# Performance work log

Measured on AMD Instinct MI355X. Metric: run time of the kernel, lower is better.

The kernel has to match this reference:

```python
import jax, jax.numpy as jnp
import numpy as np

BS, N, E = 16, 1024, 262144
IN_DIM, HID, OUT, NREL, NBASES = 3072, 512, 128, 8, 4
N_LAYERS = 3


def setup_inputs() -> dict:
    key = jax.random.key(0)
    ks = jax.random.split(key, 10)
    tot = BS * N
    return {
        "h": jax.random.normal(ks[0], (BS, N, IN_DIM), jnp.float32),
        "src": jax.random.randint(ks[1], (E,), 0, tot, jnp.int32),
        "dst": jax.random.randint(ks[2], (E,), 0, tot, jnp.int32),
        "r": jax.random.randint(ks[3], (E,), 0, NREL, jnp.int32),
        "norm": jax.random.uniform(ks[4], (E,), jnp.float32),
        "W_elmo": jax.random.normal(ks[5], (IN_DIM, 256), jnp.float32) * 0.02,
        "b_elmo": jnp.zeros((256,), jnp.float32),
        "comp": jax.random.normal(ks[6], (NREL, NBASES), jnp.float32),
        "V": jax.random.normal(ks[7], (NBASES, HID, HID), jnp.float32) * 0.04,
        "b_gcn": jnp.zeros((HID,), jnp.float32),
        "W_out": jax.random.normal(ks[8], (HID, OUT), jnp.float32) * 0.04,
        "b_out": jnp.zeros((OUT,), jnp.float32),
    }


def reference(h, src, dst, r, norm, W_elmo, b_elmo, comp, V, b_gcn, W_out, b_out):
    bs, n, _ = h.shape
    tot = bs * n
    # elmo_fnn + relu, then concat with zeros -> gnn_h_dim = 512
    x = jax.nn.relu(h @ W_elmo + b_elmo)                 # [bs, N, 256]
    x = jnp.concatenate([x, jnp.zeros_like(x)], axis=-1)  # [bs, N, 512]
    x = x.reshape(tot, HID)                               # flattened batched-graph nodes

    coef = comp[r]  # [E, NBASES] per-edge relation coefficients (basis decomposition)
    nb = V.shape[0]
    for _ in range(N_LAYERS):  # shared RelGraphConv applied repeatedly
        hs = x[src]  # [E, HID] gather source node features per edge
        # message m_e = h_src @ (sum_b comp[r_e, b] * V_b); loop over small fixed basis count
        msg = coef[:, 0:1] * (hs @ V[0])
        for b in range(1, nb):
            msg = msg + coef[:, b:b + 1] * (hs @ V[b])
        msg = msg * norm[:, None]  # per-edge norm weighting
        x = jax.ops.segment_sum(msg, dst, num_segments=tot)  # scatter-aggregate to dst
        x = jax.nn.relu(x + b_gcn)  # bias + activation (no self-loop, dropout=0)

    x = x.reshape(bs, n, HID).mean(axis=1)  # mean over nodes per graph
    logits = x @ W_out + b_out
    return jax.nn.softmax(logits, axis=-1)
```

## Files before the change

kernel.cpp:

```cpp
#include <hip/hip_runtime.h>

typedef unsigned short u16;
typedef unsigned int   u32;
typedef u16   u16x4 __attribute__((ext_vector_type(4)));
typedef u16   u16x8 __attribute__((ext_vector_type(8)));
typedef short s16x8 __attribute__((ext_vector_type(8)));
typedef u32   u32x4 __attribute__((ext_vector_type(4)));
typedef float f32x4 __attribute__((ext_vector_type(4)));

__device__ __forceinline__ float bf2f(u16 u) {
    u32 x = ((u32)u) << 16;
    return __builtin_bit_cast(float, x);
}
__device__ __forceinline__ u16 f2bf(float f) {
    u32 u = __builtin_bit_cast(u32, f);
    u32 r = u + 0x7FFFu + ((u >> 16) & 1u);
    return (u16)(r >> 16);
}
__device__ __forceinline__ u32 cvtpk(float a, float b) {
    u32 r;
    asm("v_cvt_pk_bf16_f32 %0, %1, %2" : "=v"(r) : "v"(a), "v"(b));
    return r;
}

__device__ __forceinline__ void gload16(const void* g, void* lds) {
    __builtin_amdgcn_global_load_lds((const __attribute__((address_space(1))) void*)g,
                                     (__attribute__((address_space(3))) void*)lds, 16, 0, 0);
}

#define TOT   16384
#define HID   512
#define NRELS 8
#define EDGES 262144
#define INDIM 3072
#define NOUT  128
#define NGRAPH 16
#define NODESPER 1024
#define EKSPLIT 4

#define OFF_XB     ((size_t)0)
#define OFF_Y      (OFF_XB + 16777216)
#define OFF_WCT    (OFF_Y + 134217728)
#define OFF_WET    (OFF_WCT + 4194304)
#define OFF_CNT    (OFF_WET + 1572864)
#define OFF_ROWPTR (OFF_CNT + 65536)
#define OFF_CURSOR (OFF_ROWPTR + 65552)
#define OFF_EPK    (OFF_CURSOR + 65536)
#define OFF_ENORM  (OFF_EPK + 1048576)
#define OFF_PART   (OFF_ENORM + 1048576)

__global__ __launch_bounds__(256) void k_prep_wcat(const float* __restrict__ comp,
                                                   const float* __restrict__ V,
                                                   u16* __restrict__ WcatT) {
    __shared__ float tile[64][65];
    const int r = blockIdx.z, k0 = blockIdx.x * 64, n0 = blockIdx.y * 64;
    const float c0 = comp[r * 4], c1 = comp[r * 4 + 1], c2 = comp[r * 4 + 2], c3 = comp[r * 4 + 3];
    const int tn = threadIdx.x & 63;
    const int tk = threadIdx.x >> 6;
#pragma unroll
    for (int i = 0; i < 16; ++i) {
        int k = tk + i * 4;
        const float* vp = V + (size_t)(k0 + k) * 512 + n0 + tn;
        tile[k][tn] = c0 * vp[0] + c1 * vp[262144] + c2 * vp[2 * 262144] + c3 * vp[3 * 262144];
    }
    __syncthreads();
    const int kk = threadIdx.x & 63;
#pragma unroll
    for (int i = 0; i < 16; ++i) {
        int n = (threadIdx.x >> 6) + i * 4;
        WcatT[((size_t)(r * 512 + n0 + n) << 9) + k0 + kk] = f2bf(tile[kk][n]);
    }
}

__global__ __launch_bounds__(256) void k_prep_welmo(const float* __restrict__ W,
                                                    u16* __restrict__ WT) {
    __shared__ float tile[64][65];
    const int k0 = blockIdx.x * 64, n0 = blockIdx.y * 64;
    const int tn = threadIdx.x & 63;
    const int tk = threadIdx.x >> 6;
#pragma unroll
    for (int i = 0; i < 16; ++i) {
        int k = tk + i * 4;
        tile[k][tn] = W[(size_t)(k0 + k) * 256 + n0 + tn];
    }
    __syncthreads();
    const int kk = threadIdx.x & 63;
#pragma unroll
    for (int i = 0; i < 16; ++i) {
        int n = (threadIdx.x >> 6) + i * 4;
        WT[(size_t)(n0 + n) * 3072 + k0 + kk] = f2bf(tile[kk][n]);
    }
}

__global__ __launch_bounds__(256) void k_hist(const int* __restrict__ dst, int* __restrict__ cnt) {
    int e = blockIdx.x * 256 + threadIdx.x;
    atomicAdd(&cnt[dst[e]], 1);
}

__global__ __launch_bounds__(1024) void k_scan(const int* __restrict__ cnt,
                                               int* __restrict__ rowptr,
                                               int* __restrict__ cursor) {
    __shared__ int part[1024];
    int t = threadIdx.x;
    int loc[16];
    int s = 0;
    int base = t * 16;
#pragma unroll
    for (int i = 0; i < 16; ++i) { loc[i] = s; s += cnt[base + i]; }
    part[t] = s;
    __syncthreads();
    for (int off = 1; off < 1024; off <<= 1) {
        int v = (t >= off) ? part[t - off] : 0;
        __syncthreads();
        part[t] += v;
        __syncthreads();
    }
    int excl = (t == 0) ? 0 : part[t - 1];
#pragma unroll
    for (int i = 0; i < 16; ++i) {
        int v = excl + loc[i];
        rowptr[base + i] = v;
        cursor[base + i] = v;
    }
    if (t == 1023) rowptr[TOT] = part[1023];
}

__global__ __launch_bounds__(256) void k_scatter(const int* __restrict__ src,
                                                 const int* __restrict__ dst,
                                                 const int* __restrict__ rel,
                                                 const float* __restrict__ norm,
                                                 int* __restrict__ cursor,
                                                 int* __restrict__ epk,
                                                 float* __restrict__ enorm) {
    int e = blockIdx.x * 256 + threadIdx.x;
    int d = dst[e];
    int pos = atomicAdd(&cursor[d], 1);
    epk[pos] = (src[e] << 3) | rel[e];
    enorm[pos] = norm[e];
}

__global__ __launch_bounds__(256, 4) void k_gemm(const u16* __restrict__ A,
                                                 const u16* __restrict__ BT,
                                                 u16* __restrict__ C,
                                                 int K, int lda, int ldb, int ldc) {
    __shared__ __align__(16) u16 As[128 * 64];
    __shared__ __align__(16) u16 Bs[128 * 64];

    const int t = threadIdx.x;
    const int lin = blockIdx.y * 128 + blockIdx.x;
    const int xcd = lin & 7, q = lin >> 3;
    const int tileM = (xcd * 16 + (q >> 5)) * 128;
    const int tileN = (q & 31) * 128;

    const int w = t >> 6, l = t & 63;
    const int wr = w >> 1, wc = w & 1;
    const int lo = l & 15, hi = l >> 4;

    const int srow8 = l >> 3;
    const int scol = ((l & 7) ^ srow8) * 8;

    f32x4 acc[4][4];
#pragma unroll
    for (int m = 0; m < 4; ++m)
#pragma unroll
        for (int n = 0; n < 4; ++n) acc[m][n] = f32x4{0.f, 0.f, 0.f, 0.f};

    for (int k0 = 0; k0 < K; k0 += 64) {
#pragma unroll
        for (int i = 0; i < 4; ++i) {
            const int rowblk = (w * 4 + i) * 8;
            gload16(A + (size_t)(tileM + rowblk + srow8) * lda + k0 + scol, &As[rowblk * 64]);
            gload16(BT + (size_t)(tileN + rowblk + srow8) * ldb + k0 + scol, &Bs[rowblk * 64]);
        }
        __syncthreads();

#pragma unroll
        for (int kk = 0; kk < 2; ++kk) {
            s16x8 af[4], bf[4];
#pragma unroll
            for (int m = 0; m < 4; ++m) {
                int row = wr * 64 + m * 16 + lo;
                int boff = (row * 128 + kk * 64 + hi * 16) ^ ((row & 7) << 4);
                af[m] = *(const s16x8*)((const char*)As + boff);
            }
#pragma unroll
            for (int n = 0; n < 4; ++n) {
                int row = wc * 64 + n * 16 + lo;
                int boff = (row * 128 + kk * 64 + hi * 16) ^ ((row & 7) << 4);
                bf[n] = *(const s16x8*)((const char*)Bs + boff);
            }
#pragma unroll
            for (int m = 0; m < 4; ++m)
#pragma unroll
                for (int n = 0; n < 4; ++n)
                    acc[m][n] = __builtin_amdgcn_mfma_f32_16x16x32_bf16(
                        af[m], bf[n], acc[m][n], 0, 0, 0);
        }
        __syncthreads();
    }

#pragma unroll
    for (int m = 0; m < 4; ++m)
#pragma unroll
        for (int n = 0; n < 4; ++n) {
            int col = tileN + wc * 64 + n * 16 + lo;
#pragma unroll
            for (int j = 0; j < 4; ++j) {
                int row = tileM + wr * 64 + m * 16 + hi * 4 + j;
                C[(size_t)row * ldc + col] = f2bf(acc[m][n][j]);
            }
        }
}

__global__ __launch_bounds__(256, 2) void k_gemm_elmo(const float* __restrict__ A,
                                                      const u16* __restrict__ BT,
                                                      float* __restrict__ Cp) {
    __shared__ __align__(16) float As[128 * 64];
    __shared__ __align__(16) u16   Bs[256 * 64];

    const int t = threadIdx.x;
    const int tileM = blockIdx.x * 128;
    const int kz = blockIdx.y;
    const int kbeg = kz * (INDIM / EKSPLIT);

    const int w = t >> 6, l = t & 63;
    const int wr = w >> 1, wc = w & 1;
    const int lo = l & 15, hi = l >> 4;

    const int ar = l >> 4;
    const int br = l >> 3;
    const int bcol = ((l & 7) ^ br) * 8;

    f32x4 acc[4][8];
#pragma unroll
    for (int m = 0; m < 4; ++m)
#pragma unroll
        for (int n = 0; n < 8; ++n) acc[m][n] = f32x4{0.f, 0.f, 0.f, 0.f};

    for (int ks = 0; ks < 12; ++ks) {
        const int k0 = kbeg + ks * 64;
#pragma unroll
        for (int i = 0; i < 8; ++i) {
            const int RA = (w * 8 + i) * 4;
            const int ca = (l & 15) ^ ((RA & 15) + ar);
            gload16(A + (size_t)(tileM + RA + ar) * INDIM + k0 + ca * 4, &As[RA * 64]);
            const int RB = (w * 8 + i) * 8;
            gload16(BT + (size_t)(RB + br) * INDIM + k0 + bcol, &Bs[RB * 64]);
        }
        __syncthreads();

#pragma unroll
        for (int kk = 0; kk < 2; ++kk) {
            s16x8 afr[4], bfr[8];
#pragma unroll
            for (int m = 0; m < 4; ++m) {
                int ra = wr * 64 + m * 16 + lo;
                int x0 = kk * 8 + hi * 2;
                const char* base = (const char*)As + ra * 256;
                f32x4 p = *(const f32x4*)(base + (((x0) ^ (ra & 15)) << 4));
                f32x4 q = *(const f32x4*)(base + (((x0 + 1) ^ (ra & 15)) << 4));
                u32x4 pk = {cvtpk(p[0], p[1]), cvtpk(p[2], p[3]),
                            cvtpk(q[0], q[1]), cvtpk(q[2], q[3])};
                afr[m] = __builtin_bit_cast(s16x8, pk);
            }
#pragma unroll
            for (int n = 0; n < 8; ++n) {
                int rb = wc * 128 + n * 16 + lo;
                int boff = (rb * 128 + kk * 64 + hi * 16) ^ ((rb & 7) << 4);
                bfr[n] = *(const s16x8*)((const char*)Bs + boff);
            }
#pragma unroll
            for (int m = 0; m < 4; ++m)
#pragma unroll
                for (int n = 0; n < 8; ++n)
                    acc[m][n] = __builtin_amdgcn_mfma_f32_16x16x32_bf16(
                        afr[m], bfr[n], acc[m][n], 0, 0, 0);
        }
        __syncthreads();
    }

    float* cp = Cp + (size_t)kz * TOT * 256;
#pragma unroll
    for (int m = 0; m < 4; ++m)
#pragma unroll
        for (int n = 0; n < 8; ++n) {
            int col = wc * 128 + n * 16 + lo;
#pragma unroll
            for (int j = 0; j < 4; ++j) {
                int row = tileM + wr * 64 + m * 16 + hi * 4 + j;
                cp[(size_t)row * 256 + col] = acc[m][n][j];
            }
        }
}

__global__ __launch_bounds__(256) void k_elmo_reduce(const float* __restrict__ Cp,
                                                     const float* __restrict__ bias,
                                                     u16* __restrict__ xb) {
    int idx = blockIdx.x * 256 + threadIdx.x;
    int row = idx >> 6;
    int c4 = (idx & 63) * 4;
    f32x4 s = *(const f32x4*)(Cp + (size_t)row * 256 + c4);
#pragma unroll
    for (int p = 1; p < EKSPLIT; ++p)
        s += *(const f32x4*)(Cp + (size_t)p * TOT * 256 + (size_t)row * 256 + c4);
    f32x4 bv = *(const f32x4*)(bias + c4);
    u16x4 o;
#pragma unroll
    for (int j = 0; j < 4; ++j) o[j] = f2bf(fmaxf(s[j] + bv[j], 0.f));
    *(u16x4*)(xb + (size_t)row * HID + c4) = o;
}

__global__ __launch_bounds__(256) void k_agg(const u16* __restrict__ y,
                                             const int* __restrict__ rowptr,
                                             const int* __restrict__ epk,
                                             const float* __restrict__ enorm,
                                             const float* __restrict__ bgcn,
                                             u16* __restrict__ xout) {
    const int wid = (blockIdx.x * 256 + threadIdx.x) >> 6;
    const int l = threadIdx.x & 63;
    const u32x4* yv = (const u32x4*)y;

    float a[8];
    {
        f32x4 b0 = *(const f32x4*)(bgcn + l * 8);
        f32x4 b1 = *(const f32x4*)(bgcn + l * 8 + 4);
#pragma unroll
        for (int j = 0; j < 4; ++j) { a[j] = b0[j]; a[j + 4] = b1[j]; }
    }

    const int beg = rowptr[wid], end = rowptr[wid + 1];
    int p = beg;
    for (; p + 4 <= end; p += 4) {
        int e0 = epk[p], e1 = epk[p + 1], e2 = epk[p + 2], e3 = epk[p + 3];
        float n0 = enorm[p], n1 = enorm[p + 1], n2 = enorm[p + 2], n3 = enorm[p + 3];
        u32x4 v0 = yv[(((size_t)(e0 >> 3)) << 9) + ((e0 & 7) << 6) + l];
        u32x4 v1 = yv[(((size_t)(e1 >> 3)) << 9) + ((e1 & 7) << 6) + l];
        u32x4 v2 = yv[(((size_t)(e2 >> 3)) << 9) + ((e2 & 7) << 6) + l];
        u32x4 v3 = yv[(((size_t)(e3 >> 3)) << 9) + ((e3 & 7) << 6) + l];
#pragma unroll
        for (int q = 0; q < 4; ++q) {
            a[2 * q]     = fmaf(n0, bf2f((u16)v0[q]), a[2 * q]);
            a[2 * q + 1] = fmaf(n0, bf2f((u16)(v0[q] >> 16)), a[2 * q + 1]);
            a[2 * q]     = fmaf(n1, bf2f((u16)v1[q]), a[2 * q]);
            a[2 * q + 1] = fmaf(n1, bf2f((u16)(v1[q] >> 16)), a[2 * q + 1]);
            a[2 * q]     = fmaf(n2, bf2f((u16)v2[q]), a[2 * q]);
            a[2 * q + 1] = fmaf(n2, bf2f((u16)(v2[q] >> 16)), a[2 * q + 1]);
            a[2 * q]     = fmaf(n3, bf2f((u16)v3[q]), a[2 * q]);
            a[2 * q + 1] = fmaf(n3, bf2f((u16)(v3[q] >> 16)), a[2 * q + 1]);
        }
    }
    for (; p < end; ++p) {
        int e0 = epk[p];
        float n0 = enorm[p];
        u32x4 v0 = yv[(((size_t)(e0 >> 3)) << 9) + ((e0 & 7) << 6) + l];
#pragma unroll
        for (int q = 0; q < 4; ++q) {
            a[2 * q]     = fmaf(n0, bf2f((u16)v0[q]), a[2 * q]);
            a[2 * q + 1] = fmaf(n0, bf2f((u16)(v0[q] >> 16)), a[2 * q + 1]);
        }
    }

    u16x8 o;
#pragma unroll
    for (int j = 0; j < 8; ++j) o[j] = f2bf(fmaxf(a[j], 0.f));
    *(u16x8*)(xout + ((size_t)wid << 9) + l * 8) = o;
}

__global__ __launch_bounds__(512) void k_mean1(const u16* __restrict__ xb,
                                               float* __restrict__ part) {
    int g = blockIdx.x >> 4, chunk = blockIdx.x & 15, t = threadIdx.x;
    const u16* base = xb + ((size_t)g * NODESPER + chunk * 64) * HID;
    float s = 0.f;
    for (int n = 0; n < 64; ++n) s += bf2f(base[(size_t)n * HID + t]);
    part[(size_t)blockIdx.x * HID + t] = s;
}

__global__ __launch_bounds__(512) void k_final2(const float* __restrict__ part,
                                                const float* __restrict__ W_out,
                                                const float* __restrict__ b_out,
                                                float* __restrict__ out) {
    int g = blockIdx.x, t = threadIdx.x;
    __shared__ float mean_s[512];
    __shared__ float lg[128];
    __shared__ float red[128];
    float s = 0.f;
#pragma unroll
    for (int c = 0; c < 16; ++c) s += part[((size_t)g * 16 + c) * HID + t];
    mean_s[t] = s * (1.0f / (float)NODESPER);
    __syncthreads();
    if (t < NOUT) {
        float a = b_out[t];
        for (int k = 0; k < HID; ++k) a = fmaf(mean_s[k], W_out[(size_t)k * NOUT + t], a);
        lg[t] = a;
        red[t] = a;
    }
    __syncthreads();
    for (int off = 64; off > 0; off >>= 1) {
        if (t < off) red[t] = fmaxf(red[t], red[t + off]);
        __syncthreads();
    }
    float mx = red[0];
    __syncthreads();
    if (t < NOUT) { float e = expf(lg[t] - mx); lg[t] = e; red[t] = e; }
    __syncthreads();
    for (int off = 64; off > 0; off >>= 1) {
        if (t < off) red[t] += red[t + off];
        __syncthreads();
    }
    if (t < NOUT) out[(size_t)g * NOUT + t] = lg[t] / red[0];
}

extern "C" void kernel_launch(void* const* d_in, const int* in_sizes, int n_in,
                              void* d_out, int out_size, void* d_ws, size_t ws_size,
                              hipStream_t stream) {
    const float* h      = (const float*)d_in[0];
    const int*   src    = (const int*)d_in[1];
    const int*   dst    = (const int*)d_in[2];
    const int*   rel    = (const int*)d_in[3];
    const float* norm   = (const float*)d_in[4];
    const float* W_elmo = (const float*)d_in[5];
    const float* b_elmo = (const float*)d_in[6];
    const float* comp   = (const float*)d_in[7];
    const float* V      = (const float*)d_in[8];
    const float* b_gcn  = (const float*)d_in[9];
    const float* W_out  = (const float*)d_in[10];
    const float* b_out  = (const float*)d_in[11];
    float* out = (float*)d_out;

    char* ws = (char*)d_ws;
    u16*   xb     = (u16*)(ws + OFF_XB);
    u16*   y      = (u16*)(ws + OFF_Y);
    float* elmoP  = (float*)(ws + OFF_Y);
    u16*   wcatT  = (u16*)(ws + OFF_WCT);
    u16*   welmoT = (u16*)(ws + OFF_WET);
    int*   cnt    = (int*)(ws + OFF_CNT);
    int*   rowptr = (int*)(ws + OFF_ROWPTR);
    int*   cursor = (int*)(ws + OFF_CURSOR);
    int*   epk    = (int*)(ws + OFF_EPK);
    float* enorm  = (float*)(ws + OFF_ENORM);
    float* part   = (float*)(ws + OFF_PART);

    hipMemsetAsync(xb, 0, (size_t)TOT * HID * 2, stream);
    hipMemsetAsync(cnt, 0, (size_t)TOT * 4, stream);

    k_prep_wcat<<<dim3(8, 8, 8), 256, 0, stream>>>(comp, V, wcatT);
    k_prep_welmo<<<dim3(48, 4), 256, 0, stream>>>(W_elmo, welmoT);

    k_hist<<<EDGES / 256, 256, 0, stream>>>(dst, cnt);
    k_scan<<<1, 1024, 0, stream>>>(cnt, rowptr, cursor);
    k_scatter<<<EDGES / 256, 256, 0, stream>>>(src, dst, rel, norm, cursor, epk, enorm);

    k_gemm_elmo<<<dim3(128, EKSPLIT), 256, 0, stream>>>(h, welmoT, elmoP);
    k_elmo_reduce<<<4096, 256, 0, stream>>>(elmoP, b_elmo, xb);

    for (int L = 0; L < 3; ++L) {
        const int Keff = (L == 0) ? 256 : 512;
        k_gemm<<<dim3(128, 32), 256, 0, stream>>>(xb, wcatT, y, Keff, HID, HID,
                                                  NRELS * HID);
        k_agg<<<TOT / 4, 256, 0, stream>>>(y, rowptr, epk, enorm, b_gcn, xb);
    }

    k_mean1<<<NGRAPH * 16, 512, 0, stream>>>(xb, part);
    k_final2<<<NGRAPH, 512, 0, stream>>>(part, W_out, b_out, out);
}
```

Measured before the change: 482.5 us.

## Widen GEMM N-tile to 256 and unroll aggregation gathers by eight

The per-layer GEMM now computes 128x256 output tiles per block, halving the grid and reusing each A tile across twice as many columns. It doubles the B shared-memory tile and the accumulator registers, with occupancy lowered to 2 blocks per CU. The aggregation kernel also issues eight edge gathers at once instead of four, to keep more memory loads in flight. The cost is higher register pressure in both kernels.

```diff
diff --git a/kernel.cpp b/kernel.cpp
--- a/kernel.cpp
+++ b/kernel.cpp
@@ -139,18 +139,18 @@
     enorm[pos] = norm[e];
 }
 
-__global__ __launch_bounds__(256, 4) void k_gemm(const u16* __restrict__ A,
+__global__ __launch_bounds__(256, 2) void k_gemm(const u16* __restrict__ A,
                                                  const u16* __restrict__ BT,
                                                  u16* __restrict__ C,
                                                  int K, int lda, int ldb, int ldc) {
     __shared__ __align__(16) u16 As[128 * 64];
-    __shared__ __align__(16) u16 Bs[128 * 64];
+    __shared__ __align__(16) u16 Bs[256 * 64];
 
     const int t = threadIdx.x;
     const int lin = blockIdx.y * 128 + blockIdx.x;
     const int xcd = lin & 7, q = lin >> 3;
-    const int tileM = (xcd * 16 + (q >> 5)) * 128;
-    const int tileN = (q & 31) * 128;
+    const int tileM = (xcd * 16 + (q >> 4)) * 128;
+    const int tileN = (q & 15) * 256;
 
     const int w = t >> 6, l = t & 63;
     const int wr = w >> 1, wc = w & 1;
@@ -159,24 +159,28 @@
     const int srow8 = l >> 3;
     const int scol = ((l & 7) ^ srow8) * 8;
 
-    f32x4 acc[4][4];
+    f32x4 acc[4][8];
 #pragma unroll
     for (int m = 0; m < 4; ++m)
 #pragma unroll
-        for (int n = 0; n < 4; ++n) acc[m][n] = f32x4{0.f, 0.f, 0.f, 0.f};
+        for (int n = 0; n < 8; ++n) acc[m][n] = f32x4{0.f, 0.f, 0.f, 0.f};
 
     for (int k0 = 0; k0 < K; k0 += 64) {
 #pragma unroll
         for (int i = 0; i < 4; ++i) {
             const int rowblk = (w * 4 + i) * 8;
             gload16(A + (size_t)(tileM + rowblk + srow8) * lda + k0 + scol, &As[rowblk * 64]);
+        }
+#pragma unroll
+        for (int i = 0; i < 8; ++i) {
+            const int rowblk = (w * 8 + i) * 8;
             gload16(BT + (size_t)(tileN + rowblk + srow8) * ldb + k0 + scol, &Bs[rowblk * 64]);
         }
         __syncthreads();
 
 #pragma unroll
         for (int kk = 0; kk < 2; ++kk) {
-            s16x8 af[4], bf[4];
+            s16x8 af[4], bf[8];
 #pragma unroll
             for (int m = 0; m < 4; ++m) {
                 int row = wr * 64 + m * 16 + lo;
@@ -184,15 +188,15 @@
                 af[m] = *(const s16x8*)((const char*)As + boff);
             }
 #pragma unroll
-            for (int n = 0; n < 4; ++n) {
-                int row = wc * 64 + n * 16 + lo;
+            for (int n = 0; n < 8; ++n) {
+                int row = wc * 128 + n * 16 + lo;
                 int boff = (row * 128 + kk * 64 + hi * 16) ^ ((row & 7) << 4);
                 bf[n] = *(const s16x8*)((const char*)Bs + boff);
             }
 #pragma unroll
             for (int m = 0; m < 4; ++m)
 #pragma unroll
-                for (int n = 0; n < 4; ++n)
+                for (int n = 0; n < 8; ++n)
                     acc[m][n] = __builtin_amdgcn_mfma_f32_16x16x32_bf16(
                         af[m], bf[n], acc[m][n], 0, 0, 0);
         }
@@ -202,8 +206,8 @@
 #pragma unroll
     for (int m = 0; m < 4; ++m)
 #pragma unroll
-        for (int n = 0; n < 4; ++n) {
-            int col = tileN + wc * 64 + n * 16 + lo;
+        for (int n = 0; n < 8; ++n) {
+            int col = tileN + wc * 128 + n * 16 + lo;
 #pragma unroll
             for (int j = 0; j < 4; ++j) {
                 int row = tileM + wr * 64 + m * 16 + hi * 4 + j;
@@ -330,33 +334,31 @@
 
     const int beg = rowptr[wid], end = rowptr[wid + 1];
     int p = beg;
-    for (; p + 4 <= end; p += 4) {
-        int e0 = epk[p], e1 = epk[p + 1], e2 = epk[p + 2], e3 = epk[p + 3];
-        float n0 = enorm[p], n1 = enorm[p + 1], n2 = enorm[p + 2], n3 = enorm[p + 3];
-        u32x4 v0 = yv[(((size_t)(e0 >> 3)) << 9) + ((e0 & 7) << 6) + l];
-        u32x4 v1 = yv[(((size_t)(e1 >> 3)) << 9) + ((e1 & 7) << 6) + l];
-        u32x4 v2 = yv[(((size_t)(e2 >> 3)) << 9) + ((e2 & 7) << 6) + l];
-        u32x4 v3 = yv[(((size_t)(e3 >> 3)) << 9) + ((e3 & 7) << 6) + l];
-#pragma unroll
-        for (int q = 0; q < 4; ++q) {
-            a[2 * q]     = fmaf(n0, bf2f((u16)v0[q]), a[2 * q]);
-            a[2 * q + 1] = fmaf(n0, bf2f((u16)(v0[q] >> 16)), a[2 * q + 1]);
-            a[2 * q]     = fmaf(n1, bf2f((u16)v1[q]), a[2 * q]);
-            a[2 * q + 1] = fmaf(n1, bf2f((u16)(v1[q] >> 16)), a[2 * q + 1]);
-            a[2 * q]     = fmaf(n2, bf2f((u16)v2[q]), a[2 * q]);
-            a[2 * q + 1] = fmaf(n2, bf2f((u16)(v2[q] >> 16)), a[2 * q + 1]);
-            a[2 * q]     = fmaf(n3, bf2f((u16)v3[q]), a[2 * q]);
-            a[2 * q + 1] = fmaf(n3, bf2f((u16)(v3[q] >> 16)), a[2 * q + 1]);
-        }
+    for (; p + 8 <= end; p += 8) {
+        u32x4 v[8];
+        float nv[8];
+#pragma unroll
+        for (int q = 0; q < 8; ++q) {
+            int e = epk[p + q];
+            nv[q] = enorm[p + q];
+            v[q] = yv[(((size_t)(e >> 3)) << 9) + ((e & 7) << 6) + l];
+        }
+#pragma unroll
+        for (int q = 0; q < 8; ++q)
+#pragma unroll
+            for (int j = 0; j < 4; ++j) {
+                a[2 * j]     = fmaf(nv[q], bf2f((u16)v[q][j]), a[2 * j]);
+                a[2 * j + 1] = fmaf(nv[q], bf2f((u16)(v[q][j] >> 16)), a[2 * j + 1]);
+            }
     }
     for (; p < end; ++p) {
         int e0 = epk[p];
         float n0 = enorm[p];
         u32x4 v0 = yv[(((size_t)(e0 >> 3)) << 9) + ((e0 & 7) << 6) + l];
 #pragma unroll
-        for (int q = 0; q < 4; ++q) {
-            a[2 * q]     = fmaf(n0, bf2f((u16)v0[q]), a[2 * q]);
-            a[2 * q + 1] = fmaf(n0, bf2f((u16)(v0[q] >> 16)), a[2 * q + 1]);
+        for (int j = 0; j < 4; ++j) {
+            a[2 * j]     = fmaf(n0, bf2f((u16)v0[j]), a[2 * j]);
+            a[2 * j + 1] = fmaf(n0, bf2f((u16)(v0[j] >> 16)), a[2 * j + 1]);
         }
     }
 
@@ -455,7 +457,7 @@
 
     for (int L = 0; L < 3; ++L) {
         const int Keff = (L == 0) ? 256 : 512;
-        k_gemm<<<dim3(128, 32), 256, 0, stream>>>(xb, wcatT, y, Keff, HID, HID,
+        k_gemm<<<dim3(128, 16), 256, 0, stream>>>(xb, wcatT, y, Keff, HID, HID,
                                                   NRELS * HID);
         k_agg<<<TOT / 4, 256, 0, stream>>>(y, rowptr, epk, enorm, b_gcn, xb);
     }
```

Result: faster. 471.8 us (-2.2%).
